# Kernel tuning notes

Measured on AMD Instinct MI355X. Metric: run time of the kernel, lower is better.

Reference implementation:

```python
import jax, jax.numpy as jnp
import numpy as np

K, D = 8, 4
LOG2PI = float(np.log(2.0 * np.pi))
TRIL_ROWS, TRIL_COLS = np.tril_indices(D)


def setup_inputs() -> dict:
    key = jax.random.key(0)
    k1, k2 = jax.random.split(key)
    M = 512
    B = 4096
    phi_dim = K + K * D + K * D * (D + 1) // 2  # 120
    phi = jax.random.normal(k1, (M, phi_dim), dtype=jnp.float32)
    X_ref = jax.random.normal(k2, (B, D), dtype=jnp.float32)
    return {"phi": phi, "X_ref": X_ref}


def reference(phi, X_ref):
    M = phi.shape[0]
    B = X_ref.shape[0]
    # unpack_phi: [pi_tilde | mu | L_vecs]
    pi_tilde = phi[:, :K]                                   # [M, K]
    mu = phi[:, K:K + K * D].reshape(M, K, D)               # [M, K, D]
    L_vecs = phi[:, K + K * D:].reshape(M, K, D * (D + 1) // 2)
    # L_vec_to_matrix: lower-triangular fill (row-major tril order)
    L = jnp.zeros((M, K, D, D), phi.dtype).at[:, :, TRIL_ROWS, TRIL_COLS].set(L_vecs)
    pi = jax.nn.softmax(pi_tilde, axis=-1)                  # [M, K]

    # --- mean responsibilities (GMM E-step) ---
    diff = X_ref[None, None, :, :] - mu[:, :, None, :]      # [M, K, B, D]
    L_flat = L.reshape(M * K, D, D)
    diff_flat = jnp.transpose(diff.reshape(M * K, B, D), (0, 2, 1))  # [MK, D, B]
    alpha = jax.scipy.linalg.solve_triangular(L_flat, diff_flat, lower=True)
    maha = (alpha ** 2).sum(1).reshape(M, K, B)             # Mahalanobis distances
    log_det = 2.0 * jnp.log(
        jnp.clip(jnp.abs(jnp.diagonal(L_flat, axis1=-2, axis2=-1)), 1e-8)
    ).sum(-1).reshape(M, K)
    log_norm = -0.5 * (D * LOG2PI + log_det[:, :, None])
    log_gauss = log_norm - 0.5 * maha                       # [M, K, B]
    log_joint = jnp.log(jnp.clip(pi, 1e-8))[:, :, None] + log_gauss
    log_resp = log_joint - jax.scipy.special.logsumexp(log_joint, axis=1, keepdims=True)
    resp = jnp.exp(log_resp).mean(-1)                       # [M, K]

    # --- combined embedding: [mu | log|diag L| | pi | resp] ---
    mu_flat = mu.reshape(M, K * D)
    L_diag = jnp.diagonal(L, axis1=-2, axis2=-1)            # [M, K, D]
    log_L_flat = jnp.log(jnp.clip(jnp.abs(L_diag), 1e-6)).reshape(M, K * D)
    z = jnp.concatenate([mu_flat, log_L_flat, pi, resp], axis=-1)

    # per-feature standardization across particles (torch.std => ddof=1)
    mean = z.mean(axis=0, keepdims=True)
    std = jnp.clip(z.std(axis=0, ddof=1, keepdims=True), 1e-6)
    return (z - mean) / std
```

## Files before the change

### kernel.cpp

```cpp
#include <hip/hip_runtime.h>
#include <math.h>

#define KK 8
#define LOG2E   1.4426950408889634f
#define HL2E    0.7213475204444817f
#define LN2     0.6931471805599453f
#define LOG2PI  1.8378770664093453f
#define C2CONST 5.3029936094f
#define L2CLIP8 -26.575424759f

__global__ __launch_bounds__(256) void gmm_main(const float* __restrict__ phi,
                                                const float* __restrict__ X,
                                                float* __restrict__ ws) {
    __shared__ float4 sp[4][KK][4];

    const int b = blockIdx.x;
    const int m = b >> 2;
    const int sub = b & 3;
    const int t = threadIdx.x;
    const int w = t >> 6;
    const int lane = t & 63;
    const float* row = phi + m * 120;

    const float4* X4 = reinterpret_cast<const float4*>(X);
    float4 xv[4];
    #pragma unroll
    for (int i = 0; i < 4; ++i) xv[i] = X4[sub * 1024 + w * 256 + i * 64 + lane];

    if (lane < KK) {
        float mx = row[0];
        #pragma unroll
        for (int j = 1; j < KK; ++j) mx = fmaxf(mx, row[j]);
        float s = 0.f;
        #pragma unroll
        for (int j = 0; j < KK; ++j)
            s += __builtin_amdgcn_exp2f((row[j] - mx) * LOG2E);
        float l2pi = fmaxf((row[lane] - mx) * LOG2E - __builtin_amdgcn_logf(s),
                           L2CLIP8);

        const float* muk = row + 8 + lane * 4;
        const float* Lv  = row + 40 + lane * 10;
        float l00 = Lv[0], l10 = Lv[1], l11 = Lv[2], l20 = Lv[3], l21 = Lv[4],
              l22 = Lv[5], l30 = Lv[6], l31 = Lv[7], l32 = Lv[8], l33 = Lv[9];
        float i0 = 1.f / l00, i1 = 1.f / l11, i2 = 1.f / l22, i3 = 1.f / l33;
        float w00 = i0;
        float w10 = -i1 * l10 * w00;
        float w11 = i1;
        float w20 = -i2 * (l20 * w00 + l21 * w10);
        float w21 = -i2 * (l21 * w11);
        float w22 = i2;
        float w30 = -i3 * (l30 * w00 + l31 * w10 + l32 * w20);
        float w31 = -i3 * (l31 * w11 + l32 * w21);
        float w32 = -i3 * (l32 * w22);
        float w33 = i3;
        float sl = __builtin_amdgcn_logf(fmaxf(fabsf(l00), 1e-8f)) +
                   __builtin_amdgcn_logf(fmaxf(fabsf(l11), 1e-8f)) +
                   __builtin_amdgcn_logf(fmaxf(fabsf(l22), 1e-8f)) +
                   __builtin_amdgcn_logf(fmaxf(fabsf(l33), 1e-8f));
        float c2 = l2pi - C2CONST - sl;
        sp[w][lane][0] = make_float4(muk[0], muk[1], muk[2], muk[3]);
        sp[w][lane][1] = make_float4(w00, w10, w11, w20);
        sp[w][lane][2] = make_float4(w21, w22, w30, w31);
        sp[w][lane][3] = make_float4(w32, w33, c2, 0.f);
    }

    float acc[KK];
    #pragma unroll
    for (int k = 0; k < KK; ++k) acc[k] = 0.f;

    float lj[4][KK];
    #pragma unroll
    for (int k = 0; k < KK; ++k) {
        float4 p0 = sp[w][k][0], p1 = sp[w][k][1],
               p2 = sp[w][k][2], p3 = sp[w][k][3];
        #pragma unroll
        for (int i = 0; i < 4; ++i) {
            float d0 = xv[i].x - p0.x;
            float d1 = xv[i].y - p0.y;
            float d2 = xv[i].z - p0.z;
            float d3 = xv[i].w - p0.w;
            float a0 = d0 * p1.x;
            float a1 = fmaf(p1.y, d0, d1 * p1.z);
            float a2 = fmaf(p1.w, d0, fmaf(p2.x, d1, d2 * p2.y));
            float a3 = fmaf(p2.z, d0, fmaf(p2.w, d1, fmaf(p3.x, d2, d3 * p3.y)));
            float sq = fmaf(a0, a0, fmaf(a1, a1, fmaf(a2, a2, a3 * a3)));
            lj[i][k] = fmaf(-HL2E, sq, p3.z);
        }
    }
    #pragma unroll
    for (int i = 0; i < 4; ++i) {
        float mx = lj[i][0];
        #pragma unroll
        for (int k = 1; k < KK; ++k) mx = fmaxf(mx, lj[i][k]);
        float e[KK], s = 0.f;
        #pragma unroll
        for (int k = 0; k < KK; ++k) {
            e[k] = __builtin_amdgcn_exp2f(lj[i][k] - mx);
            s += e[k];
        }
        float inv = __builtin_amdgcn_rcpf(s);
        #pragma unroll
        for (int k = 0; k < KK; ++k) acc[k] = fmaf(e[k], inv, acc[k]);
    }

    #pragma unroll
    for (int k = 0; k < KK; ++k) {
        float v = acc[k];
        #pragma unroll
        for (int off = 32; off; off >>= 1) v += __shfl_xor(v, off, 64);
        acc[k] = v;
    }
    if (lane < KK) {
        int p = m * 16 + sub * 4 + w;
        ws[p * 8 + lane] = acc[lane];
    }
}

__global__ __launch_bounds__(512) void gmm_norm(const float* __restrict__ phi,
                                                const float* __restrict__ ws,
                                                float* __restrict__ out, int M) {
    __shared__ float sw[8];
    const int col = blockIdx.x;
    const int t = threadIdx.x;
    const float* row = phi + t * 120;

    float v;
    if (col < 32) {
        v = row[8 + col];
    } else if (col < 64) {
        int j = col - 32, k = j >> 2, d = j & 3;
        int didx = (d == 0) ? 0 : (d == 1) ? 2 : (d == 2) ? 5 : 9;
        v = __builtin_amdgcn_logf(fmaxf(fabsf(row[40 + k * 10 + didx]), 1e-6f)) * LN2;
    } else if (col < 72) {
        int k = col - 64;
        float mx = row[0];
        #pragma unroll
        for (int j = 1; j < KK; ++j) mx = fmaxf(mx, row[j]);
        float s = 0.f;
        #pragma unroll
        for (int j = 0; j < KK; ++j)
            s += __builtin_amdgcn_exp2f((row[j] - mx) * LOG2E);
        v = __builtin_amdgcn_exp2f((row[k] - mx) * LOG2E) *
            __builtin_amdgcn_rcpf(s);
    } else {
        int k = col - 72;
        v = 0.f;
        #pragma unroll
        for (int q = 0; q < 16; ++q) v += ws[(t * 16 + q) * 8 + k];
    }

    float r = v;
    #pragma unroll
    for (int off = 32; off; off >>= 1) r += __shfl_xor(r, off, 64);
    if ((t & 63) == 0) sw[t >> 6] = r;
    __syncthreads();
    float tot = 0.f;
    #pragma unroll
    for (int w = 0; w < 8; ++w) tot += sw[w];
    float mean = tot / (float)M;
    __syncthreads();

    float d = v - mean;
    r = d * d;
    #pragma unroll
    for (int off = 32; off; off >>= 1) r += __shfl_xor(r, off, 64);
    if ((t & 63) == 0) sw[t >> 6] = r;
    __syncthreads();
    float tot2 = 0.f;
    #pragma unroll
    for (int w = 0; w < 8; ++w) tot2 += sw[w];
    float stdv = fmaxf(sqrtf(tot2 / (float)(M - 1)), 1e-6f);

    out[t * 80 + col] = d / stdv;
}

extern "C" void kernel_launch(void* const* d_in, const int* in_sizes, int n_in,
                              void* d_out, int out_size, void* d_ws, size_t ws_size,
                              hipStream_t stream) {
    const float* phi = (const float*)d_in[0];
    const float* X   = (const float*)d_in[1];
    const int M = in_sizes[0] / 120;
    float* ws = (float*)d_ws;

    gmm_main<<<M * 4, 256, 0, stream>>>(phi, X, ws);
    gmm_norm<<<80, 512, 0, stream>>>(phi, ws, (float*)d_out, M);
}
```

Measured before the change: 73.94 us.

## Split per-component parameter precompute into a setup kernel shared across blocks

Adds a gmm_setup kernel that computes the softmax, inverse Cholesky factors and log-normalisers once per (particle, component) into workspace, and writes the non-responsibility embedding columns straight into the output. gmm_main then reads the precomputed parameters from global memory instead of having each wave recompute them and sync through shared memory. gmm_norm reads those columns back and uses a transposed partial-sum layout so its loads coalesce. This removes redundant per-wave setup work at the cost of an extra kernel launch and a global round-trip.

```diff
diff --git a/kernel.cpp b/kernel.cpp
--- a/kernel.cpp
+++ b/kernel.cpp
@@ -5,64 +5,84 @@
 #define LOG2E   1.4426950408889634f
 #define HL2E    0.7213475204444817f
 #define LN2     0.6931471805599453f
-#define LOG2PI  1.8378770664093453f
 #define C2CONST 5.3029936094f
 #define L2CLIP8 -26.575424759f
 
-__global__ __launch_bounds__(256) void gmm_main(const float* __restrict__ phi,
+
+__global__ __launch_bounds__(256) void gmm_setup(const float* __restrict__ phi,
+                                                 float* __restrict__ ws,
+                                                 float* __restrict__ z) {
+    const int tid = blockIdx.x * 256 + threadIdx.x;
+    const int m = tid >> 3, k = tid & 7;
+    const float* row = phi + m * 120;
+
+    float mx = row[0];
+    #pragma unroll
+    for (int j = 1; j < KK; ++j) mx = fmaxf(mx, row[j]);
+    float s = 0.f;
+    #pragma unroll
+    for (int j = 0; j < KK; ++j)
+        s += __builtin_amdgcn_exp2f((row[j] - mx) * LOG2E);
+    float l2s = __builtin_amdgcn_logf(s);
+    float pik = __builtin_amdgcn_exp2f((row[k] - mx) * LOG2E) *
+                __builtin_amdgcn_rcpf(s);
+    float l2pi = fmaxf((row[k] - mx) * LOG2E - l2s, L2CLIP8);
+
+    const float* muk = row + 8 + k * 4;
+    const float* Lv  = row + 40 + k * 10;
+    float l00 = Lv[0], l10 = Lv[1], l11 = Lv[2], l20 = Lv[3], l21 = Lv[4],
+          l22 = Lv[5], l30 = Lv[6], l31 = Lv[7], l32 = Lv[8], l33 = Lv[9];
+    float i0 = 1.f / l00, i1 = 1.f / l11, i2 = 1.f / l22, i3 = 1.f / l33;
+    float w00 = i0;
+    float w10 = -i1 * l10 * w00;
+    float w11 = i1;
+    float w20 = -i2 * (l20 * w00 + l21 * w10);
+    float w21 = -i2 * (l21 * w11);
+    float w22 = i2;
+    float w30 = -i3 * (l30 * w00 + l31 * w10 + l32 * w20);
+    float w31 = -i3 * (l31 * w11 + l32 * w21);
+    float w32 = -i3 * (l32 * w22);
+    float w33 = i3;
+    float sl = __builtin_amdgcn_logf(fmaxf(fabsf(l00), 1e-8f)) +
+               __builtin_amdgcn_logf(fmaxf(fabsf(l11), 1e-8f)) +
+               __builtin_amdgcn_logf(fmaxf(fabsf(l22), 1e-8f)) +
+               __builtin_amdgcn_logf(fmaxf(fabsf(l33), 1e-8f));
+    float c2 = l2pi - C2CONST - sl;
+
+    float4* P = reinterpret_cast<float4*>(ws) + tid * 4;
+    P[0] = make_float4(muk[0], muk[1], muk[2], muk[3]);
+    P[1] = make_float4(w00, w10, w11, w20);
+    P[2] = make_float4(w21, w22, w30, w31);
+    P[3] = make_float4(w32, w33, c2, 0.f);
+
+    float* zr = z + m * 80;
+    #pragma unroll
+    for (int d = 0; d < 4; ++d) zr[k * 4 + d] = muk[d];
+    zr[32 + k * 4 + 0] = __builtin_amdgcn_logf(fmaxf(fabsf(l00), 1e-6f)) * LN2;
+    zr[32 + k * 4 + 1] = __builtin_amdgcn_logf(fmaxf(fabsf(l11), 1e-6f)) * LN2;
+    zr[32 + k * 4 + 2] = __builtin_amdgcn_logf(fmaxf(fabsf(l22), 1e-6f)) * LN2;
+    zr[32 + k * 4 + 3] = __builtin_amdgcn_logf(fmaxf(fabsf(l33), 1e-6f)) * LN2;
+    zr[64 + k] = pik;
+}
+
+__global__ __launch_bounds__(256) void gmm_main(const float* __restrict__ ws,
                                                 const float* __restrict__ X,
-                                                float* __restrict__ ws) {
-    __shared__ float4 sp[4][KK][4];
-
+                                                float* __restrict__ part,
+                                                int M) {
     const int b = blockIdx.x;
     const int m = b >> 2;
     const int sub = b & 3;
     const int t = threadIdx.x;
     const int w = t >> 6;
     const int lane = t & 63;
-    const float* row = phi + m * 120;
 
     const float4* X4 = reinterpret_cast<const float4*>(X);
     float4 xv[4];
     #pragma unroll
-    for (int i = 0; i < 4; ++i) xv[i] = X4[sub * 1024 + w * 256 + i * 64 + lane];
+    for (int i = 0; i < 4; ++i)
+        xv[i] = X4[sub * 1024 + w * 256 + i * 64 + lane];
 
-    if (lane < KK) {
-        float mx = row[0];
-        #pragma unroll
-        for (int j = 1; j < KK; ++j) mx = fmaxf(mx, row[j]);
-        float s = 0.f;
-        #pragma unroll
-        for (int j = 0; j < KK; ++j)
-            s += __builtin_amdgcn_exp2f((row[j] - mx) * LOG2E);
-        float l2pi = fmaxf((row[lane] - mx) * LOG2E - __builtin_amdgcn_logf(s),
-                           L2CLIP8);
-
-        const float* muk = row + 8 + lane * 4;
-        const float* Lv  = row + 40 + lane * 10;
-        float l00 = Lv[0], l10 = Lv[1], l11 = Lv[2], l20 = Lv[3], l21 = Lv[4],
-              l22 = Lv[5], l30 = Lv[6], l31 = Lv[7], l32 = Lv[8], l33 = Lv[9];
-        float i0 = 1.f / l00, i1 = 1.f / l11, i2 = 1.f / l22, i3 = 1.f / l33;
-        float w00 = i0;
-        float w10 = -i1 * l10 * w00;
-        float w11 = i1;
-        float w20 = -i2 * (l20 * w00 + l21 * w10);
-        float w21 = -i2 * (l21 * w11);
-        float w22 = i2;
-        float w30 = -i3 * (l30 * w00 + l31 * w10 + l32 * w20);
-        float w31 = -i3 * (l31 * w11 + l32 * w21);
-        float w32 = -i3 * (l32 * w22);
-        float w33 = i3;
-        float sl = __builtin_amdgcn_logf(fmaxf(fabsf(l00), 1e-8f)) +
-                   __builtin_amdgcn_logf(fmaxf(fabsf(l11), 1e-8f)) +
-                   __builtin_amdgcn_logf(fmaxf(fabsf(l22), 1e-8f)) +
-                   __builtin_amdgcn_logf(fmaxf(fabsf(l33), 1e-8f));
-        float c2 = l2pi - C2CONST - sl;
-        sp[w][lane][0] = make_float4(muk[0], muk[1], muk[2], muk[3]);
-        sp[w][lane][1] = make_float4(w00, w10, w11, w20);
-        sp[w][lane][2] = make_float4(w21, w22, w30, w31);
-        sp[w][lane][3] = make_float4(w32, w33, c2, 0.f);
-    }
+    const float4* Pm = reinterpret_cast<const float4*>(ws) + m * 32;
 
     float acc[KK];
     #pragma unroll
@@ -71,8 +91,8 @@
     float lj[4][KK];
     #pragma unroll
     for (int k = 0; k < KK; ++k) {
-        float4 p0 = sp[w][k][0], p1 = sp[w][k][1],
-               p2 = sp[w][k][2], p3 = sp[w][k][3];
+        float4 p0 = Pm[k * 4 + 0], p1 = Pm[k * 4 + 1],
+               p2 = Pm[k * 4 + 2], p3 = Pm[k * 4 + 3];
         #pragma unroll
         for (int i = 0; i < 4; ++i) {
             float d0 = xv[i].x - p0.x;
@@ -111,42 +131,25 @@
         acc[k] = v;
     }
     if (lane < KK) {
-        int p = m * 16 + sub * 4 + w;
-        ws[p * 8 + lane] = acc[lane];
+        int p = sub * 4 + w;
+        part[(p * KK + lane) * M + m] = acc[lane];
     }
 }
 
-__global__ __launch_bounds__(512) void gmm_norm(const float* __restrict__ phi,
-                                                const float* __restrict__ ws,
-                                                float* __restrict__ out, int M) {
+__global__ __launch_bounds__(512) void gmm_norm(const float* __restrict__ part,
+                                                float* __restrict__ z, int M) {
     __shared__ float sw[8];
     const int col = blockIdx.x;
     const int t = threadIdx.x;
-    const float* row = phi + t * 120;
 
     float v;
-    if (col < 32) {
-        v = row[8 + col];
-    } else if (col < 64) {
-        int j = col - 32, k = j >> 2, d = j & 3;
-        int didx = (d == 0) ? 0 : (d == 1) ? 2 : (d == 2) ? 5 : 9;
-        v = __builtin_amdgcn_logf(fmaxf(fabsf(row[40 + k * 10 + didx]), 1e-6f)) * LN2;
-    } else if (col < 72) {
-        int k = col - 64;
-        float mx = row[0];
-        #pragma unroll
-        for (int j = 1; j < KK; ++j) mx = fmaxf(mx, row[j]);
-        float s = 0.f;
-        #pragma unroll
-        for (int j = 0; j < KK; ++j)
-            s += __builtin_amdgcn_exp2f((row[j] - mx) * LOG2E);
-        v = __builtin_amdgcn_exp2f((row[k] - mx) * LOG2E) *
-            __builtin_amdgcn_rcpf(s);
+    if (col < 72) {
+        v = z[t * 80 + col];
     } else {
         int k = col - 72;
         v = 0.f;
         #pragma unroll
-        for (int q = 0; q < 16; ++q) v += ws[(t * 16 + q) * 8 + k];
+        for (int q = 0; q < 16; ++q) v += part[(q * KK + k) * M + t];
     }
 
     float r = v;
@@ -171,7 +174,7 @@
     for (int w = 0; w < 8; ++w) tot2 += sw[w];
     float stdv = fmaxf(sqrtf(tot2 / (float)(M - 1)), 1e-6f);
 
-    out[t * 80 + col] = d / stdv;
+    z[t * 80 + col] = d / stdv;
 }
 
 extern "C" void kernel_launch(void* const* d_in, const int* in_sizes, int n_in,
@@ -180,8 +183,11 @@
     const float* phi = (const float*)d_in[0];
     const float* X   = (const float*)d_in[1];
     const int M = in_sizes[0] / 120;
-    float* ws = (float*)d_ws;
+    float* ws   = (float*)d_ws;
+    float* part = ws + 65536;
+    float* z    = (float*)d_out;
 
-    gmm_main<<<M * 4, 256, 0, stream>>>(phi, X, ws);
-    gmm_norm<<<80, 512, 0, stream>>>(phi, ws, (float*)d_out, M);
+    gmm_setup<<<(M * KK) / 256, 256, 0, stream>>>(phi, ws, z);
+    gmm_main<<<M * 4, 256, 0, stream>>>(ws, X, part, M);
+    gmm_norm<<<80, 512, 0, stream>>>(part, z, M);
 }
```

Measured after the change: 72.63 us. No clear change (-1.8%).
